# Kernel optimization log

Measured on AMD Instinct MI355X. Metric: run time of the kernel, lower is better.

The kernel has to match this reference:

```python
import jax, jax.numpy as jnp
import numpy as np

DIM = 512
CHUNK = 64
LN_EPS = 1e-5


def setup_inputs() -> dict:
    key = jax.random.key(0)
    ks = jax.random.split(key, 9)
    B, S, D = 4, 4096, DIM
    x = jax.random.normal(ks[0], (B, S, D), dtype=jnp.float32)
    # Linear weights stored as [in, out] (equivalent to torch W.T)
    W_omega = jax.random.normal(ks[1], (D, D), dtype=jnp.float32) / np.sqrt(D)
    b_omega = jnp.zeros((D,), dtype=jnp.float32)
    log_scale = jnp.full((D,), np.log(0.1), dtype=jnp.float32)
    ln_gamma = jnp.ones((4 * D,), dtype=jnp.float32)
    ln_beta = jnp.zeros((4 * D,), dtype=jnp.float32)
    W1 = jax.random.normal(ks[2], (4 * D, 2 * D), dtype=jnp.float32) / np.sqrt(4 * D)
    b1 = jnp.zeros((2 * D,), dtype=jnp.float32)
    W2 = jax.random.normal(ks[3], (2 * D, D), dtype=jnp.float32) / np.sqrt(2 * D)
    b2 = jnp.zeros((D,), dtype=jnp.float32)
    return {"x": x, "W_omega": W_omega, "b_omega": b_omega, "log_scale": log_scale,
            "ln_gamma": ln_gamma, "ln_beta": ln_beta, "W1": W1, "b1": b1, "W2": W2, "b2": b2}


def reference(x, W_omega, b_omega, log_scale, ln_gamma, ln_beta, W1, b1, W2, b2):
    B, S, D = x.shape
    C = CHUNK
    # S chosen as multiple of C, so pad_len == 0 (matches torch no-pad branch)
    N = S // C
    omega = x @ W_omega + b_omega                      # [B,S,D]
    oc = omega.reshape(B, N, C, D)
    xc = x.reshape(B, N, C, D)
    pos = jnp.arange(1, C + 1, dtype=x.dtype)          # [C]
    pos_scale = (1.0 / jnp.sqrt(pos))[None, None, :, None]
    scale = jnp.exp(log_scale)
    phi = jnp.cumsum(oc * scale * pos_scale, axis=2)   # [B,N,C,D]
    cos_phi = jnp.cos(phi)
    sin_phi = jnp.sin(phi)
    cr = xc * cos_phi                                   # content modulated real
    ci = xc * sin_phi                                   # content modulated imag
    pos_norm = pos[None, None, :, None]
    mr = jnp.cumsum(cr, axis=2) / pos_norm              # memory real
    mi = jnp.cumsum(ci, axis=2) / pos_norm              # memory imag
    rr = mr * cos_phi + mi * sin_phi                    # retrieved real
    ri = mi * cos_phi - mr * sin_phi                    # retrieved imag
    ctx = jnp.concatenate([cr.reshape(B, S, D), ci.reshape(B, S, D),
                           rr.reshape(B, S, D), ri.reshape(B, S, D)], axis=-1)  # [B,S,4D]
    mu = jnp.mean(ctx, axis=-1, keepdims=True)
    var = jnp.mean((ctx - mu) ** 2, axis=-1, keepdims=True)
    h = (ctx - mu) / jnp.sqrt(var + LN_EPS) * ln_gamma + ln_beta
    h = h @ W1 + b1
    h = jax.nn.gelu(h, approximate=False)               # torch GELU default = exact erf
    out = h @ W2 + b2                                   # dropout is identity at eval
    return x + out
```

## Files before the change

kernel.cpp:

```cpp
#include <hip/hip_runtime.h>
#include <hip/hip_bf16.h>
#include <math.h>


typedef __bf16 bf16x8 __attribute__((ext_vector_type(8)));
typedef __bf16 bf16x4 __attribute__((ext_vector_type(4)));
typedef __bf16 bf16x2 __attribute__((ext_vector_type(2)));
typedef float  f32x4  __attribute__((ext_vector_type(4)));

typedef __attribute__((address_space(1))) void* gas_ptr;
typedef __attribute__((address_space(3))) void* las_ptr;

__device__ __forceinline__ void load_lds16(const void* g, void* l) {
    __builtin_amdgcn_global_load_lds((gas_ptr)g, (las_ptr)l, 16, 0, 0);
}

__device__ __forceinline__ void transpose_tile(const float* __restrict__ in,
                                               __bf16* __restrict__ out,
                                               int K, int N, int bx, int by,
                                               float (*tile)[33])
{
    const int tid = threadIdx.x;
    const int tx = tid & 31, ty = tid >> 5;
    const int n0 = bx * 32, k0 = by * 32;
    #pragma unroll
    for (int i = 0; i < 32; i += 8)
        tile[ty + i][tx] = in[(size_t)(k0 + ty + i) * N + n0 + tx];
    __syncthreads();
    #pragma unroll
    for (int i = 0; i < 32; i += 8)
        out[(size_t)(n0 + ty + i) * K + k0 + tx] = (__bf16)tile[tx][ty + i];
}

__global__ __launch_bounds__(256)
void prep_kernel(const float* __restrict__ x, __bf16* __restrict__ xb,
                 const float* __restrict__ W_omega, __bf16* __restrict__ womT,
                 const float* __restrict__ W1, __bf16* __restrict__ w1T,
                 const float* __restrict__ W2, __bf16* __restrict__ w2T)
{
    __shared__ float tile[32][33];
    const int bid = blockIdx.x;
    if (bid < 8192) {
        int i = bid * 256 + threadIdx.x;
        float4 v = ((const float4*)x)[i];
        bf16x4 o = { (__bf16)v.x, (__bf16)v.y, (__bf16)v.z, (__bf16)v.w };
        ((bf16x4*)xb)[i] = o;
    } else if (bid < 8448) {
        int t = bid - 8192;
        transpose_tile(W_omega, womT, 512, 512, t & 15, t >> 4, tile);
    } else if (bid < 10496) {
        int t = bid - 8448;
        transpose_tile(W1, w1T, 2048, 1024, t & 31, t >> 5, tile);
    } else {
        int t = bid - 10496;
        transpose_tile(W2, w2T, 1024, 512, t & 15, t >> 4, tile);
    }
}

template<int MODE>
__global__ __launch_bounds__(256)
void gemm_kernel(const __bf16* __restrict__ A, const __bf16* __restrict__ Bt,
                 const float* __restrict__ bias, const __bf16* __restrict__ resid,
                 void* __restrict__ out, int M, int N, int K)
{
    __shared__ __bf16 As[2][128 * 64];
    __shared__ __bf16 Bs[2][128 * 64];

    const int tid     = threadIdx.x;
    const int tiles_n = N >> 7;
    const int ln_tn   = __ffs(tiles_n) - 1;
    const int per_m   = (M >> 7) >> 3;

    const int xcd = blockIdx.x & 7;
    const int j   = blockIdx.x >> 3;
    const int tile_m = (xcd * per_m + (j >> ln_tn)) << 7;
    const int tile_n = (j & (tiles_n - 1)) << 7;

    const int wave = tid >> 6;
    const int lane = tid & 63;

    const int srow = lane >> 3;
    const int scol = ((lane & 7) ^ srow) << 3;

    const __bf16* Ags = A  + (size_t)(tile_m + wave * 32 + srow) * K + scol;
    const __bf16* Bgs = Bt + (size_t)(tile_n + wave * 32 + srow) * K + scol;

    const int m0 = (wave >> 1) << 6;
    const int n0 = (wave & 1) << 6;
    const int lr = lane & 15;
    const int q  = lane >> 4;
    const int l7 = lane & 7;
    const int fc0 = ((0 + q) ^ l7) << 3;
    const int fc1 = ((4 + q) ^ l7) << 3;

    f32x4 acc[4][4];
    #pragma unroll
    for (int i = 0; i < 4; ++i)
        #pragma unroll
        for (int jj = 0; jj < 4; ++jj)
            acc[i][jj] = (f32x4){0.f, 0.f, 0.f, 0.f};

    const int nIter = K >> 6;

    #pragma unroll
    for (int c = 0; c < 4; ++c) {
        load_lds16(Ags + (size_t)(c * 8) * K, &As[0][(wave * 32 + c * 8) * 64]);
        load_lds16(Bgs + (size_t)(c * 8) * K, &Bs[0][(wave * 32 + c * 8) * 64]);
    }

    for (int it = 0; it < nIter; ++it) {
        const int cur = it & 1;
        __syncthreads();
        if (it + 1 < nIter) {
            const int nk = (it + 1) << 6;
            #pragma unroll
            for (int c = 0; c < 4; ++c) {
                load_lds16(Ags + nk + (size_t)(c * 8) * K, &As[cur ^ 1][(wave * 32 + c * 8) * 64]);
                load_lds16(Bgs + nk + (size_t)(c * 8) * K, &Bs[cur ^ 1][(wave * 32 + c * 8) * 64]);
            }
        }

        const __bf16* as = As[cur];
        const __bf16* bs = Bs[cur];
        {
            bf16x8 af[4], bq[4];
            #pragma unroll
            for (int i = 0; i < 4; ++i)
                af[i] = *(const bf16x8*)&as[(m0 + i * 16 + lr) * 64 + fc0];
            #pragma unroll
            for (int jj = 0; jj < 4; ++jj)
                bq[jj] = *(const bf16x8*)&bs[(n0 + jj * 16 + lr) * 64 + fc0];
            #pragma unroll
            for (int i = 0; i < 4; ++i)
                #pragma unroll
                for (int jj = 0; jj < 4; ++jj)
                    acc[i][jj] = __builtin_amdgcn_mfma_f32_16x16x32_bf16(af[i], bq[jj], acc[i][jj], 0, 0, 0);
        }
        {
            bf16x8 af[4], bq[4];
            #pragma unroll
            for (int i = 0; i < 4; ++i)
                af[i] = *(const bf16x8*)&as[(m0 + i * 16 + lr) * 64 + fc1];
            #pragma unroll
            for (int jj = 0; jj < 4; ++jj)
                bq[jj] = *(const bf16x8*)&bs[(n0 + jj * 16 + lr) * 64 + fc1];
            #pragma unroll
            for (int i = 0; i < 4; ++i)
                #pragma unroll
                for (int jj = 0; jj < 4; ++jj)
                    acc[i][jj] = __builtin_amdgcn_mfma_f32_16x16x32_bf16(af[i], bq[jj], acc[i][jj], 0, 0, 0);
        }
    }

    const int orow0 = tile_m + m0 + (q << 2);
    const int ocol0 = tile_n + n0 + lr;
    #pragma unroll
    for (int i = 0; i < 4; ++i) {
        #pragma unroll
        for (int jj = 0; jj < 4; ++jj) {
            const int col = ocol0 + jj * 16;
            const float bv = bias[col];
            #pragma unroll
            for (int r = 0; r < 4; ++r) {
                const int row = orow0 + i * 16 + r;
                float v = acc[i][jj][r] + bv;
                size_t idx = (size_t)row * N + col;
                if (MODE == 0) {
                    ((__bf16*)out)[idx] = (__bf16)v;
                } else if (MODE == 1) {
                    float g = 0.5f * v * (1.0f + erff(v * 0.70710678118654752f));
                    ((__bf16*)out)[idx] = (__bf16)g;
                } else {
                    ((float*)out)[idx] = v + (float)resid[idx];
                }
            }
        }
    }
}

template<int MODE>
__global__ __launch_bounds__(512, 1)
void gemm256_kernel(const __bf16* __restrict__ A, const __bf16* __restrict__ Bt,
                    const float* __restrict__ bias, void* __restrict__ out,
                    int M, int N, int K)
{
    __shared__ __bf16 As[4][256 * 32];
    __shared__ __bf16 Bs[4][256 * 32];

    const int tid  = threadIdx.x;
    const int wv   = tid >> 6;
    const int lane = tid & 63;
    const int wm   = wv >> 2;
    const int wn   = wv & 3;

    const int tiles_n = N >> 8;
    const int ln_tn   = __ffs(tiles_n) - 1;
    const int per_m   = (M >> 8) >> 3;

    const int xcd = blockIdx.x & 7;
    const int j   = blockIdx.x >> 3;
    const int tile_m = (xcd * per_m + (j >> ln_tn)) << 8;
    const int tile_n = (j & (tiles_n - 1)) << 8;

    const int srow = 16 * wv + (lane >> 2);
    const int sig8 = (((lane & 3) ^ ((lane >> 3) & 3)) << 3);

    const __bf16* Ag = A  + (size_t)(tile_m + srow) * K + sig8;
    const __bf16* Bg = Bt + (size_t)(tile_n + srow) * K + sig8;
    const size_t rowK128 = (size_t)128 * K;
    const int lbase = wv * 512;

    const int lr    = lane & 15;
    const int q4    = lane >> 4;
    const int fslot = ((q4 ^ ((lane >> 1) & 3)) << 3);
    const int arow0 = wm * 128 + lr;
    const int brow0 = wn * 64 + lr;

    const unsigned ldsA0 = (unsigned)(size_t)(las_ptr)&As[0][0];
    const unsigned ldsB0 = (unsigned)(size_t)(las_ptr)&Bs[0][0];
    const unsigned asA = ldsA0 + (unsigned)((arow0 * 32 + fslot) << 1);
    const unsigned asB = ldsB0 + (unsigned)((brow0 * 32 + fslot) << 1);

    f32x4 acc[8][4];
    #pragma unroll
    for (int i = 0; i < 8; ++i)
        #pragma unroll
        for (int jj = 0; jj < 4; ++jj)
            acc[i][jj] = (f32x4){0.f, 0.f, 0.f, 0.f};

    const int NKS = K >> 5;

    auto stage = [&](int ks) {
        const int slot = ks & 3;
        const __bf16* ag = Ag + (ks << 5);
        const __bf16* bg = Bg + (ks << 5);
        load_lds16(ag,           &As[slot][lbase]);
        load_lds16(ag + rowK128, &As[slot][4096 + lbase]);
        load_lds16(bg,           &Bs[slot][lbase]);
        load_lds16(bg + rowK128, &Bs[slot][4096 + lbase]);
    };

    bf16x8 afA[8], bqA[4], afB[8], bqB[4];

#define DSR(d, a, o) asm volatile("ds_read_b128 %0, %1 offset:" o \
                                  : "=v"(d) : "v"(a))
#define SB __builtin_amdgcn_sched_barrier(0)
#define MM4(CAF, CBQ, I)                                                      \
    acc[I][0] = __builtin_amdgcn_mfma_f32_16x16x32_bf16(CAF[I], CBQ[0], acc[I][0], 0, 0, 0); \
    acc[I][1] = __builtin_amdgcn_mfma_f32_16x16x32_bf16(CAF[I], CBQ[1], acc[I][1], 0, 0, 0); \
    acc[I][2] = __builtin_amdgcn_mfma_f32_16x16x32_bf16(CAF[I], CBQ[2], acc[I][2], 0, 0, 0); \
    acc[I][3] = __builtin_amdgcn_mfma_f32_16x16x32_bf16(CAF[I], CBQ[3], acc[I][3], 0, 0, 0);

#define G256_READ(KS, NAF, NBQ)                                               \
    {                                                                         \
        const unsigned aA_ = asA + (unsigned)(((KS) & 3) << 14);              \
        const unsigned aB_ = asB + (unsigned)(((KS) & 3) << 14);              \
        DSR(NAF[0], aA_, "0");    DSR(NAF[1], aA_, "1024");                   \
        DSR(NAF[2], aA_, "2048"); DSR(NAF[3], aA_, "3072");                   \
        DSR(NAF[4], aA_, "4096"); DSR(NAF[5], aA_, "5120");                   \
        DSR(NAF[6], aA_, "6144"); DSR(NAF[7], aA_, "7168");                   \
        DSR(NBQ[0], aB_, "0");    DSR(NBQ[1], aB_, "1024");                   \
        DSR(NBQ[2], aB_, "2048"); DSR(NBQ[3], aB_, "3072");                   \
    }

#define G256_PHASE_FULL(KS, CAF, CBQ, NAF, NBQ)                               \
    {                                                                         \
        const int ks_ = (KS);                                                 \
        asm volatile("s_waitcnt vmcnt(8)" ::: "memory");                      \
        __builtin_amdgcn_s_barrier();                                         \
        asm volatile("" ::: "memory");                                        \
        const int slot_ = (ks_ + 4) & 3;                                      \
        const __bf16* ag_ = Ag + ((ks_ + 4) << 5);                            \
        const __bf16* bg_ = Bg + ((ks_ + 4) << 5);                            \
        const unsigned aA_ = asA + (unsigned)(((ks_ + 1) & 3) << 14);         \
        const unsigned aB_ = asB + (unsigned)(((ks_ + 1) & 3) << 14);         \
        __builtin_amdgcn_s_setprio(1);                                        \
        load_lds16(ag_,           &As[slot_][lbase]);                         \
        MM4(CAF, CBQ, 0) SB;                                                  \
        load_lds16(ag_ + rowK128, &As[slot_][4096 + lbase]);                  \
        MM4(CAF, CBQ, 1) SB;                                                  \
        load_lds16(bg_,           &Bs[slot_][lbase]);                         \
        MM4(CAF, CBQ, 2) SB;                                                  \
        load_lds16(bg_ + rowK128, &Bs[slot_][4096 + lbase]);                  \
        MM4(CAF, CBQ, 3) SB;                                                  \
        DSR(NAF[0], aA_, "0"); DSR(NAF[1], aA_, "1024");                      \
        DSR(NAF[2], aA_, "2048");                                             \
        MM4(CAF, CBQ, 4) SB;                                                  \
        DSR(NAF[3], aA_, "3072"); DSR(NAF[4], aA_, "4096");                   \
        DSR(NAF[5], aA_, "5120");                                             \
        MM4(CAF, CBQ, 5) SB;                                                  \
        DSR(NAF[6], aA_, "6144"); DSR(NAF[7], aA_, "7168");                   \
        DSR(NBQ[0], aB_, "0");                                                \
        MM4(CAF, CBQ, 6) SB;                                                  \
        DSR(NBQ[1], aB_, "1024"); DSR(NBQ[2], aB_, "2048");                   \
        DSR(NBQ[3], aB_, "3072");                                             \
        MM4(CAF, CBQ, 7)                                                      \
        __builtin_amdgcn_s_setprio(0);                                        \
        asm volatile("s_waitcnt lgkmcnt(0)" ::: "memory");                    \
        __builtin_amdgcn_sched_barrier(0);                                    \
    }

#define G256_PHASE_TAIL(KS, CAF, CBQ, NAF, NBQ)                               \
    {                                                                         \
        const int ks_ = (KS);                                                 \
        const int r_  = NKS - 1 - ks_;                                        \
        if (r_ >= 3)      asm volatile("s_waitcnt vmcnt(8)" ::: "memory");    \
        else if (r_ == 2) asm volatile("s_waitcnt vmcnt(4)" ::: "memory");    \
        else if (r_ == 1) asm volatile("s_waitcnt vmcnt(0)" ::: "memory");    \
        __builtin_amdgcn_s_barrier();                                         \
        asm volatile("" ::: "memory");                                        \
        if (ks_ + 4 < NKS) stage(ks_ + 4);                                    \
        if (ks_ + 1 < NKS) G256_READ(ks_ + 1, NAF, NBQ)                       \
        __builtin_amdgcn_s_setprio(1);                                        \
        _Pragma("unroll")                                                     \
        for (int i_ = 0; i_ < 8; ++i_)                                        \
            _Pragma("unroll")                                                 \
            for (int j_ = 0; j_ < 4; ++j_)                                    \
                acc[i_][j_] = __builtin_amdgcn_mfma_f32_16x16x32_bf16(        \
                    CAF[i_], CBQ[j_], acc[i_][j_], 0, 0, 0);                  \
        __builtin_amdgcn_s_setprio(0);                                        \
        asm volatile("s_waitcnt lgkmcnt(0)" ::: "memory");                    \
        __builtin_amdgcn_sched_barrier(0);                                    \
    }

    stage(0); stage(1); stage(2);
    asm volatile("s_waitcnt vmcnt(8)" ::: "memory");
    __builtin_amdgcn_s_barrier();
    asm volatile("" ::: "memory");
    stage(3);
    G256_READ(0, afA, bqA)
    asm volatile("s_waitcnt lgkmcnt(0)" ::: "memory");
    __builtin_amdgcn_sched_barrier(0);

    int ks = 0;
    for (; ks + 6 < NKS; ks += 2) {
        G256_PHASE_FULL(ks,     afA, bqA, afB, bqB)
        G256_PHASE_FULL(ks + 1, afB, bqB, afA, bqA)
    }
    for (; ks < NKS; ks += 2) {
        G256_PHASE_TAIL(ks,     afA, bqA, afB, bqB)
        G256_PHASE_TAIL(ks + 1, afB, bqB, afA, bqA)
    }

#undef G256_PHASE_FULL
#undef G256_PHASE_TAIL
#undef G256_READ
#undef MM4
#undef SB
#undef DSR

    const int orow0 = tile_m + wm * 128 + (q4 << 2);
    const int ocol0 = tile_n + wn * 64 + lr;
    #pragma unroll
    for (int i = 0; i < 8; ++i) {
        #pragma unroll
        for (int jj = 0; jj < 4; ++jj) {
            const int col = ocol0 + jj * 16;
            const float bv = bias[col];
            #pragma unroll
            for (int r = 0; r < 4; ++r) {
                const int row = orow0 + i * 16 + r;
                float v = acc[i][jj][r] + bv;
                if (MODE == 1) {
                    float g = 0.5f * v * (1.0f + erff(v * 0.70710678118654752f));
                    ((__bf16*)out)[(size_t)row * N + col] = (__bf16)g;
                } else {
                    ((__bf16*)out)[(size_t)row * N + col] = (__bf16)v;
                }
            }
        }
    }
}

__global__ __launch_bounds__(512)
void scan_ln_kernel(const __bf16* __restrict__ xb, const __bf16* __restrict__ omega,
                    const float* __restrict__ log_scale,
                    const float* __restrict__ gamma, const float* __restrict__ beta,
                    __bf16* __restrict__ ctx)
{
    const int chunk = blockIdx.x;
    const int d     = threadIdx.x;
    const int lane  = d & 63, wv = d >> 6;
    const size_t base = (size_t)chunk * 64 * 512;

    const float scale = expf(log_scale[d]);
    const float g0 = gamma[d], g1 = gamma[512 + d], g2 = gamma[1024 + d], g3 = gamma[1536 + d];
    const float e0 = beta[d],  e1 = beta[512 + d],  e2 = beta[1024 + d],  e3 = beta[1536 + d];

    float phi = 0.f, scr = 0.f, sci = 0.f;
    __shared__ float red[2][16];

    float om_n = (float)omega[base + d];
    float xv_n = (float)xb[base + d];

    for (int c = 0; c < 64; ++c) {
        const float om = om_n;
        const float xv = xv_n;
        if (c < 63) {
            om_n = (float)omega[base + (size_t)(c + 1) * 512 + d];
            xv_n = (float)xb[base + (size_t)(c + 1) * 512 + d];
        }
        phi += om * scale * rsqrtf((float)(c + 1));
        float sp, cp;
        __sincosf(phi, &sp, &cp);
        const float cr = xv * cp, ci = xv * sp;
        scr += cr; sci += ci;
        const float inv = 1.0f / (float)(c + 1);
        const float mr = scr * inv, mi = sci * inv;
        const float rr = mr * cp + mi * sp;
        const float ri = mi * cp - mr * sp;

        float s  = cr + ci + rr + ri;
        float s2 = cr * cr + ci * ci + rr * rr + ri * ri;
        #pragma unroll
        for (int o = 32; o > 0; o >>= 1) {
            s  += __shfl_down(s, o);
            s2 += __shfl_down(s2, o);
        }
        if (lane == 0) { red[c & 1][wv] = s; red[c & 1][8 + wv] = s2; }
        __syncthreads();
        float S = 0.f, S2 = 0.f;
        #pragma unroll
        for (int i = 0; i < 8; ++i) { S += red[c & 1][i]; S2 += red[c & 1][8 + i]; }
        const float mu   = S * (1.0f / 2048.0f);
        const float var  = S2 * (1.0f / 2048.0f) - mu * mu;
        const float rstd = rsqrtf(var + 1e-5f);

        const size_t ob = ((size_t)chunk * 64 + c) * 2048;
        ctx[ob + d]        = (__bf16)(((cr - mu) * rstd) * g0 + e0);
        ctx[ob + 512 + d]  = (__bf16)(((ci - mu) * rstd) * g1 + e1);
        ctx[ob + 1024 + d] = (__bf16)(((rr - mu) * rstd) * g2 + e2);
        ctx[ob + 1536 + d] = (__bf16)(((ri - mu) * rstd) * g3 + e3);
    }
}

extern "C" void kernel_launch(void* const* d_in, const int* in_sizes, int n_in,
                              void* d_out, int out_size, void* d_ws, size_t ws_size,
                              hipStream_t stream)
{
    const float* x         = (const float*)d_in[0];
    const float* W_omega   = (const float*)d_in[1];
    const float* b_omega   = (const float*)d_in[2];
    const float* log_scale = (const float*)d_in[3];
    const float* ln_gamma  = (const float*)d_in[4];
    const float* ln_beta   = (const float*)d_in[5];
    const float* W1        = (const float*)d_in[6];
    const float* b1        = (const float*)d_in[7];
    const float* W2        = (const float*)d_in[8];
    const float* b2        = (const float*)d_in[9];
    float* out = (float*)d_out;

    char* ws = (char*)d_ws;
    __bf16* xb    = (__bf16*)(ws);
    __bf16* womT  = (__bf16*)(ws + 16777216);
    __bf16* w1T   = (__bf16*)(ws + 17301504);
    __bf16* w2T   = (__bf16*)(ws + 21495808);
    __bf16* omega = (__bf16*)(ws + 22544384);
    __bf16* hbuf  = (__bf16*)(ws + 22544384);
    __bf16* ctx   = (__bf16*)(ws + 56098816);

    prep_kernel<<<11008, 256, 0, stream>>>(x, xb, W_omega, womT, W1, w1T, W2, w2T);

    gemm_kernel<0><<<512, 256, 0, stream>>>(xb, womT, b_omega, nullptr, omega, 16384, 512, 512);

    scan_ln_kernel<<<256, 512, 0, stream>>>(xb, omega, log_scale, ln_gamma, ln_beta, ctx);

    gemm256_kernel<1><<<256, 512, 0, stream>>>(ctx, w1T, b1, hbuf, 16384, 1024, 2048);

    gemm_kernel<2><<<512, 256, 0, stream>>>(hbuf, w2T, b2, xb, out, 16384, 512, 1024);
}
```

Measured before the change: 266.8 us.

## Run scan+LayerNorm with one wavefront per chunk and 8 features per lane

Restructures the chunk scan kernel so a single 64-lane wavefront processes a chunk, each lane handling 8 contiguous features with vectorized bf16x8 loads and stores. The LayerNorm reduction becomes a pure wave shuffle reduction, removing the per-step shared-memory exchange and block barrier. This trades away thread-level parallelism (one wave per block, 256 waves total) for less synchronization and wider memory accesses, which may hurt latency hiding.

```diff
diff --git a/kernel.cpp b/kernel.cpp
--- a/kernel.cpp
+++ b/kernel.cpp
@@ -372,65 +372,82 @@
     }
 }
 
-__global__ __launch_bounds__(512)
+__global__ __launch_bounds__(64)
 void scan_ln_kernel(const __bf16* __restrict__ xb, const __bf16* __restrict__ omega,
                     const float* __restrict__ log_scale,
                     const float* __restrict__ gamma, const float* __restrict__ beta,
                     __bf16* __restrict__ ctx)
 {
     const int chunk = blockIdx.x;
-    const int d     = threadIdx.x;
-    const int lane  = d & 63, wv = d >> 6;
+    const int lane  = threadIdx.x;
+    const int d0    = lane << 3;
     const size_t base = (size_t)chunk * 64 * 512;
 
-    const float scale = expf(log_scale[d]);
-    const float g0 = gamma[d], g1 = gamma[512 + d], g2 = gamma[1024 + d], g3 = gamma[1536 + d];
-    const float e0 = beta[d],  e1 = beta[512 + d],  e2 = beta[1024 + d],  e3 = beta[1536 + d];
-
-    float phi = 0.f, scr = 0.f, sci = 0.f;
-    __shared__ float red[2][16];
-
-    float om_n = (float)omega[base + d];
-    float xv_n = (float)xb[base + d];
+    float scale[8], g0[8], g1[8], g2[8], g3[8], e0[8], e1[8], e2[8], e3[8];
+    #pragma unroll
+    for (int u = 0; u < 8; ++u) {
+        const int d = d0 + u;
+        scale[u] = expf(log_scale[d]);
+        g0[u] = gamma[d]; g1[u] = gamma[512 + d]; g2[u] = gamma[1024 + d]; g3[u] = gamma[1536 + d];
+        e0[u] = beta[d];  e1[u] = beta[512 + d];  e2[u] = beta[1024 + d];  e3[u] = beta[1536 + d];
+    }
+
+    float phi[8], scr[8], sci[8];
+    #pragma unroll
+    for (int u = 0; u < 8; ++u) { phi[u] = 0.f; scr[u] = 0.f; sci[u] = 0.f; }
+
+    bf16x8 om_n = *(const bf16x8*)&omega[base + d0];
+    bf16x8 xv_n = *(const bf16x8*)&xb[base + d0];
 
     for (int c = 0; c < 64; ++c) {
-        const float om = om_n;
-        const float xv = xv_n;
+        const bf16x8 omv = om_n;
+        const bf16x8 xvv = xv_n;
         if (c < 63) {
-            om_n = (float)omega[base + (size_t)(c + 1) * 512 + d];
-            xv_n = (float)xb[base + (size_t)(c + 1) * 512 + d];
-        }
-        phi += om * scale * rsqrtf((float)(c + 1));
-        float sp, cp;
-        __sincosf(phi, &sp, &cp);
-        const float cr = xv * cp, ci = xv * sp;
-        scr += cr; sci += ci;
+            om_n = *(const bf16x8*)&omega[base + (size_t)(c + 1) * 512 + d0];
+            xv_n = *(const bf16x8*)&xb[base + (size_t)(c + 1) * 512 + d0];
+        }
+        const float rsq = rsqrtf((float)(c + 1));
         const float inv = 1.0f / (float)(c + 1);
-        const float mr = scr * inv, mi = sci * inv;
-        const float rr = mr * cp + mi * sp;
-        const float ri = mi * cp - mr * sp;
-
-        float s  = cr + ci + rr + ri;
-        float s2 = cr * cr + ci * ci + rr * rr + ri * ri;
+
+        float cr[8], ci[8], rr[8], ri[8];
+        float s = 0.f, s2 = 0.f;
+        #pragma unroll
+        for (int u = 0; u < 8; ++u) {
+            const float om = (float)omv[u];
+            const float xv = (float)xvv[u];
+            phi[u] += om * scale[u] * rsq;
+            float sp, cp;
+            __sincosf(phi[u], &sp, &cp);
+            cr[u] = xv * cp; ci[u] = xv * sp;
+            scr[u] += cr[u]; sci[u] += ci[u];
+            const float mr = scr[u] * inv, mi = sci[u] * inv;
+            rr[u] = mr * cp + mi * sp;
+            ri[u] = mi * cp - mr * sp;
+            s  += cr[u] + ci[u] + rr[u] + ri[u];
+            s2 += cr[u]*cr[u] + ci[u]*ci[u] + rr[u]*rr[u] + ri[u]*ri[u];
+        }
         #pragma unroll
         for (int o = 32; o > 0; o >>= 1) {
-            s  += __shfl_down(s, o);
-            s2 += __shfl_down(s2, o);
-        }
-        if (lane == 0) { red[c & 1][wv] = s; red[c & 1][8 + wv] = s2; }
-        __syncthreads();
-        float S = 0.f, S2 = 0.f;
-        #pragma unroll
-        for (int i = 0; i < 8; ++i) { S += red[c & 1][i]; S2 += red[c & 1][8 + i]; }
-        const float mu   = S * (1.0f / 2048.0f);
-        const float var  = S2 * (1.0f / 2048.0f) - mu * mu;
+            s  += __shfl_xor(s, o);
+            s2 += __shfl_xor(s2, o);
+        }
+        const float mu   = s * (1.0f / 2048.0f);
+        const float var  = s2 * (1.0f / 2048.0f) - mu * mu;
         const float rstd = rsqrtf(var + 1e-5f);
 
         const size_t ob = ((size_t)chunk * 64 + c) * 2048;
-        ctx[ob + d]        = (__bf16)(((cr - mu) * rstd) * g0 + e0);
-        ctx[ob + 512 + d]  = (__bf16)(((ci - mu) * rstd) * g1 + e1);
-        ctx[ob + 1024 + d] = (__bf16)(((rr - mu) * rstd) * g2 + e2);
-        ctx[ob + 1536 + d] = (__bf16)(((ri - mu) * rstd) * g3 + e3);
+        bf16x8 o0, o1, o2, o3;
+        #pragma unroll
+        for (int u = 0; u < 8; ++u) {
+            o0[u] = (__bf16)(((cr[u] - mu) * rstd) * g0[u] + e0[u]);
+            o1[u] = (__bf16)(((ci[u] - mu) * rstd) * g1[u] + e1[u]);
+            o2[u] = (__bf16)(((rr[u] - mu) * rstd) * g2[u] + e2[u]);
+            o3[u] = (__bf16)(((ri[u] - mu) * rstd) * g3[u] + e3[u]);
+        }
+        *(bf16x8*)&ctx[ob + d0]        = o0;
+        *(bf16x8*)&ctx[ob + 512 + d0]  = o1;
+        *(bf16x8*)&ctx[ob + 1024 + d0] = o2;
+        *(bf16x8*)&ctx[ob + 1536 + d0] = o3;
     }
 }
 
@@ -463,7 +480,7 @@
 
     gemm_kernel<0><<<512, 256, 0, stream>>>(xb, womT, b_omega, nullptr, omega, 16384, 512, 512);
 
-    scan_ln_kernel<<<256, 512, 0, stream>>>(xb, omega, log_scale, ln_gamma, ln_beta, ctx);
+    scan_ln_kernel<<<256, 64, 0, stream>>>(xb, omega, log_scale, ln_gamma, ln_beta, ctx);
 
     gemm256_kernel<1><<<256, 512, 0, stream>>>(ctx, w1T, b1, hbuf, 16384, 1024, 2048);
 
```

Result: slower. 296.7 us (+11.2%).
